# Kernel tuning notes

Hardware: AMD Instinct MI355X
Metric: run time of the kernel (lower is better)

Reference implementation:

```python
import jax, jax.numpy as jnp
import numpy as np
from jax import lax

A_RATIOS = (0.5, 1.0, 2.0)
A_SCALES = (8, 16, 32)
FEAT_STRIDE = 16
BASE_SIZE = 16
PRE_NMS = 6000     # n_test_pre_nms
POST_NMS = 300     # n_test_post_nms
NMS_THRESH = 0.7
MIN_SIZE = 16.0
SCALE = 1.0        # forward(scale=1.0) default
NEG = -1e10


def _anchor_base():
    # standard generate_anchor_base: centered at (8,8), ratios x scales
    py = px = BASE_SIZE / 2.0
    rows = []
    for r in A_RATIOS:
        for s in A_SCALES:
            h = BASE_SIZE * s * np.sqrt(r)
            w = BASE_SIZE * s * np.sqrt(1.0 / r)
            rows.append([py - h / 2.0, px - w / 2.0, py + h / 2.0, px + w / 2.0])
    return np.asarray(rows, np.float32)  # (A, 4)


def _all_anchors(height, width):
    base = jnp.asarray(_anchor_base())                                  # (A, 4)
    sy = (jnp.arange(height) * FEAT_STRIDE).astype(jnp.float32)
    sx = (jnp.arange(width) * FEAT_STRIDE).astype(jnp.float32)
    gy, gx = jnp.meshgrid(sy, sx, indexing='ij')
    shift = jnp.stack([gy.ravel(), gx.ravel(), gy.ravel(), gx.ravel()], axis=1)  # (K, 4)
    anch = base[None, :, :] + shift[:, None, :]                         # (K, A, 4)
    return anch.reshape(-1, 4)                                          # (K*A, 4)


def _conv(x, w, b, pad):
    y = lax.conv_general_dilated(x, w, (1, 1), [(pad, pad), (pad, pad)],
                                 dimension_numbers=('NCHW', 'OIHW', 'NCHW'))
    return y + b[None, :, None, None]


def _loc2bbox(anchors, locs):
    h = anchors[:, 2] - anchors[:, 0]
    w = anchors[:, 3] - anchors[:, 1]
    cy = anchors[:, 0] + 0.5 * h
    cx = anchors[:, 1] + 0.5 * w
    dy, dx, dh, dw = locs[:, 0], locs[:, 1], locs[:, 2], locs[:, 3]
    ncy = dy * h + cy
    ncx = dx * w + cx
    nh = jnp.exp(dh) * h
    nw = jnp.exp(dw) * w
    return jnp.stack([ncy - 0.5 * nh, ncx - 0.5 * nw,
                      ncy + 0.5 * nh, ncx + 0.5 * nw], axis=1)


def _iou_one_vs_all(box, boxes):
    ty = jnp.maximum(box[0], boxes[:, 0])
    tx = jnp.maximum(box[1], boxes[:, 1])
    by = jnp.minimum(box[2], boxes[:, 2])
    bx = jnp.minimum(box[3], boxes[:, 3])
    inter = jnp.maximum(by - ty, 0.0) * jnp.maximum(bx - tx, 0.0)
    a1 = (box[2] - box[0]) * (box[3] - box[1])
    a2 = (boxes[:, 2] - boxes[:, 0]) * (boxes[:, 3] - boxes[:, 1])
    return inter / (a1 + a2 - inter + 1e-9)


def _nms(boxes, scores):
    # greedy NMS with fixed POST_NMS output; invalid slots are zero boxes
    def step(s, _):
        i = jnp.argmax(s)
        valid = s[i] > NEG / 2
        ious = _iou_one_vs_all(boxes[i], boxes)
        s = jnp.where(ious > NMS_THRESH, NEG, s)  # suppresses self (iou=1)
        return s, (i, valid)
    _, (idx, valid) = lax.scan(step, scores, None, length=POST_NMS)
    return boxes[idx] * valid[:, None].astype(boxes.dtype)  # (POST_NMS, 4)


def _proposals(anchors, locs, fg, img_h, img_w):
    boxes = _loc2bbox(anchors, locs)
    boxes = jnp.stack([jnp.clip(boxes[:, 0], 0.0, img_h),
                       jnp.clip(boxes[:, 1], 0.0, img_w),
                       jnp.clip(boxes[:, 2], 0.0, img_h),
                       jnp.clip(boxes[:, 3], 0.0, img_w)], axis=1)
    hs = boxes[:, 2] - boxes[:, 0]
    ws = boxes[:, 3] - boxes[:, 1]
    ok = (hs >= MIN_SIZE * SCALE) & (ws >= MIN_SIZE * SCALE)
    sc = jnp.where(ok, fg, NEG)
    top_sc, idx = lax.top_k(sc, PRE_NMS)
    return _nms(boxes[idx], top_sc)


def reference(base_feat, W_conv1, b_conv1, W_score, b_score, W_loc, b_loc, img_h, img_w):
    N, _, H, W = base_feat.shape
    A = 9
    mid = jax.nn.relu(_conv(base_feat, W_conv1, b_conv1, 1))            # (N,512,H,W)
    rpn_locs = _conv(mid, W_loc, b_loc, 0).transpose(0, 2, 3, 1).reshape(N, H * W * A, 4)
    raw = _conv(mid, W_score, b_score, 0).transpose(0, 2, 3, 1)          # (N,H,W,2A)
    rpn_scores = raw.reshape(N, H * W * A, 2)
    fg = jax.nn.softmax(raw.reshape(N, H, W, A, 2), axis=-1)[..., 1].reshape(N, -1)
    anchors = _all_anchors(H, W)                                         # (H*W*A,4)
    ih, iw = float(img_h), float(img_w)
    prop = jax.vmap(lambda l, f: _proposals(anchors, l, f, ih, iw))(rpn_locs, fg)
    rois = prop.reshape(N * POST_NMS, 4)
    roi_indices = jnp.repeat(jnp.arange(N, dtype=jnp.int32), POST_NMS)
    return rpn_locs, rpn_scores, rois, roi_indices, anchors


def setup_inputs() -> dict:
    key = jax.random.key(0)
    k0, k1, k2, k3 = jax.random.split(key, 4)
    N, C, H, W = 4, 512, 64, 64
    nA = 9
    return {
        'base_feat': jax.random.normal(k0, (N, C, H, W), jnp.float32),
        'W_conv1': 0.01 * jax.random.normal(k1, (512, 512, 3, 3), jnp.float32),
        'b_conv1': jnp.zeros((512,), jnp.float32),
        'W_score': 0.01 * jax.random.normal(k2, (2 * nA, 512, 1, 1), jnp.float32),
        'b_score': jnp.zeros((2 * nA,), jnp.float32),
        'W_loc': 0.01 * jax.random.normal(k3, (4 * nA, 512, 1, 1), jnp.float32),
        'b_loc': jnp.zeros((4 * nA,), jnp.float32),
        'img_h': 1024,
        'img_w': 1024,
    }
```

## Files before the change

### kernel.cpp

```cpp
#include <hip/hip_runtime.h>
#include <math.h>

#define HH 64
#define WW 64
#define NIMG 4
#define CIN 512
#define AA 9
#define HWA (HH*WW*AA)
#define PRE_NMS 6000
#define POST_NMS 300
#define NEGV (-1e10f)
#define NEGK 0xD01502F9u
#define NWORD 94

#define OFF1 589824
#define OFF2 884736
#define OFF3 889536
#define OFF4 890736

typedef unsigned int u32;
typedef unsigned long long u64;
typedef _Float16 f16;
typedef _Float16 half8 __attribute__((ext_vector_type(8)));
typedef float f32x4 __attribute__((ext_vector_type(4)));

__device__ __forceinline__ void gload_lds16(const void* g, void* l)
{
    __builtin_amdgcn_global_load_lds((const __attribute__((address_space(1))) void*)g,
                                     (__attribute__((address_space(3))) void*)l,
                                     16, 0, 0);
}

__global__ __launch_bounds__(256) void k_prep_x(const float* __restrict__ x,
                                                f16* __restrict__ xh,
                                                f16* __restrict__ xl)
{
    __shared__ float tile[64][65];
    int ci0 = blockIdx.x * 64, y = blockIdx.y, n = blockIdx.z;
    int t = threadIdx.x;
    #pragma unroll
    for (int l = 0; l < 16; ++l) {
        int idx = l * 256 + t;
        int cc = idx >> 6, xc = idx & 63;
        tile[cc][xc] = x[((size_t)(n * CIN + ci0 + cc) * HH + y) * WW + xc];
    }
    __syncthreads();
    #pragma unroll
    for (int l = 0; l < 16; ++l) {
        int idx = l * 256 + t;
        int xc = idx >> 6, cc = idx & 63;
        float v = tile[cc][xc];
        f16 hi = (f16)v;
        f16 lo = (f16)(v - (float)hi);
        size_t o = ((size_t)(n * 64 + y) * 64 + xc) * 512 + ci0 + cc;
        xh[o] = hi; xl[o] = lo;
    }
}

__global__ __launch_bounds__(256) void k_prep_w(const float* __restrict__ W1,
                                                f16* __restrict__ wh,
                                                f16* __restrict__ wl)
{
    int idx = blockIdx.x * 256 + threadIdx.x;
    int co = idx >> 9, ci = idx & 511;
    #pragma unroll
    for (int tap = 0; tap < 9; ++tap) {
        float v = W1[(size_t)idx * 9 + tap];
        f16 hi = (f16)v;
        f16 lo = (f16)(v - (float)hi);
        size_t o = ((size_t)tap * 512 + co) * 512 + ci;
        wh[o] = hi; wl[o] = lo;
    }
}

__global__ __launch_bounds__(256, 4) void k_conv_mfma(const f16* __restrict__ xh,
                                                      const f16* __restrict__ xl,
                                                      const f16* __restrict__ wh,
                                                      const f16* __restrict__ wl,
                                                      const float* __restrict__ bias,
                                                      float* __restrict__ mid)
{
    __shared__ f16 sX[2][4][64][32];
    const int t = threadIdx.x;
    const int co0 = blockIdx.x * 64, yb = blockIdx.y, n = blockIdx.z;
    const int y0 = yb * 2;
    const int wv = t >> 6, lane = t & 63;
    const int q = lane >> 4, li = lane & 15;
    const int mh = wv & 1;
    const int xhp = wv >> 1;

    if (yb == 0 || yb == 31) {
        int rowu = (yb == 0) ? 0 : 3072;
        u32* p = (u32*)&sX[0][0][0][0];
        #pragma unroll
        for (int l = 0; l < 8; ++l) {
            int idx = l * 256 + t;
            int plane = idx >> 10, r = idx & 1023;
            p[plane * 4096 + rowu + r] = 0;
        }
    }

    f32x4 acc[2][2][2];
    #pragma unroll
    for (int mt = 0; mt < 2; ++mt)
        #pragma unroll
        for (int xn = 0; xn < 2; ++xn)
            #pragma unroll
            for (int yy = 0; yy < 2; ++yy)
                acc[mt][xn][yy] = (f32x4){0.f, 0.f, 0.f, 0.f};

    auto prefetch = [&](int ci0) {
        #pragma unroll
        for (int m = 0; m < 8; ++m) {
            int k2 = wv * 8 + m;
            int plane = k2 >> 4;
            int row = (k2 >> 2) & 3;
            int gy = y0 - 1 + row;
            if ((unsigned)gy < 64u) {
                int col = ((k2 & 3) << 4) + (lane >> 2);
                int s = lane & 3;
                const f16* src = (plane ? xl : xh) +
                    (((size_t)(n * 64 + gy) * 64 + col) * 512 + ci0 + s * 8);
                f16* dst = &sX[0][0][0][0] + (size_t)k2 * 512 + lane * 8;
                gload_lds16(src, dst);
            }
        }
    };

    half8 wa[2][2], wn[2][2];
    auto loadW = [&](half8 w[2][2], int ci0, int tap) {
        #pragma unroll
        for (int mt = 0; mt < 2; ++mt) {
            size_t base = ((size_t)(tap * 512) + co0 + mh * 32 + mt * 16 + li) * 512 + ci0 + q * 8;
            w[0][mt] = *(const half8*)(wh + base);
            w[1][mt] = *(const half8*)(wl + base);
        }
    };

    prefetch(0);
    loadW(wa, 0, 0);

    const half8 zero8 = {(f16)0, (f16)0, (f16)0, (f16)0, (f16)0, (f16)0, (f16)0, (f16)0};

    for (int chunk = 0; chunk < 16; ++chunk) {
        const int ci0 = chunk * 32;
        __syncthreads();

        #pragma unroll
        for (int tap = 0; tap < 9; ++tap) {
            if (tap < 8) loadW(wn, ci0, tap + 1);
            const int ky = tap / 3, kx = tap - ky * 3;

            half8 B[2][2][2];
            #pragma unroll
            for (int xn = 0; xn < 2; ++xn) {
                int xc = xhp * 32 + xn * 16 + li;
                int colr = xc + kx - 1;
                bool oob = (colr < 0) || (colr > 63);
                int colc = oob ? 0 : colr;
                #pragma unroll
                for (int yy = 0; yy < 2; ++yy) {
                    int row = yy + ky;
                    const f16* ph = &sX[0][row][colc][q * 8];
                    half8 vh = *(const half8*)ph;
                    half8 vl = *(const half8*)(ph + 8192);
                    if (oob) { vh = zero8; vl = zero8; }
                    B[0][xn][yy] = vh; B[1][xn][yy] = vl;
                }
            }
            #pragma unroll
            for (int mt = 0; mt < 2; ++mt)
                #pragma unroll
                for (int xn = 0; xn < 2; ++xn)
                    #pragma unroll
                    for (int yy = 0; yy < 2; ++yy)
                        acc[mt][xn][yy] = __builtin_amdgcn_mfma_f32_16x16x32_f16(wa[0][mt], B[0][xn][yy], acc[mt][xn][yy], 0, 0, 0);
            #pragma unroll
            for (int mt = 0; mt < 2; ++mt)
                #pragma unroll
                for (int xn = 0; xn < 2; ++xn)
                    #pragma unroll
                    for (int yy = 0; yy < 2; ++yy)
                        acc[mt][xn][yy] = __builtin_amdgcn_mfma_f32_16x16x32_f16(wa[0][mt], B[1][xn][yy], acc[mt][xn][yy], 0, 0, 0);
            #pragma unroll
            for (int mt = 0; mt < 2; ++mt)
                #pragma unroll
                for (int xn = 0; xn < 2; ++xn)
                    #pragma unroll
                    for (int yy = 0; yy < 2; ++yy)
                        acc[mt][xn][yy] = __builtin_amdgcn_mfma_f32_16x16x32_f16(wa[1][mt], B[0][xn][yy], acc[mt][xn][yy], 0, 0, 0);

            if (tap < 8) {
                #pragma unroll
                for (int pl = 0; pl < 2; ++pl)
                    #pragma unroll
                    for (int mt = 0; mt < 2; ++mt) wa[pl][mt] = wn[pl][mt];
            }
        }

        if (chunk + 1 < 16) {
            __syncthreads();
            prefetch(ci0 + 32);
            loadW(wa, ci0 + 32, 0);
        }
    }

    #pragma unroll
    for (int mt = 0; mt < 2; ++mt) {
        #pragma unroll
        for (int r = 0; r < 4; ++r) {
            int co = co0 + mh * 32 + mt * 16 + q * 4 + r;
            float bv = bias[co];
            #pragma unroll
            for (int xn = 0; xn < 2; ++xn) {
                int xc = xhp * 32 + xn * 16 + li;
                #pragma unroll
                for (int yy = 0; yy < 2; ++yy) {
                    float v = acc[mt][xn][yy][r] + bv;
                    mid[((size_t)(n * 512 + co) * HH + y0 + yy) * WW + xc] = v > 0.f ? v : 0.f;
                }
            }
        }
    }
}

__global__ __launch_bounds__(256) void k_htrans(const float* __restrict__ Ws,
                                                const float* __restrict__ Wl,
                                                float* __restrict__ Wt2)
{
    int i = blockIdx.x * 256 + threadIdx.x;
    if (i >= 512 * 64) return;
    int ci = i >> 6, co = i & 63;
    float v = 0.f;
    if (co < 18) v = Ws[co * 512 + ci];
    else if (co < 54) v = Wl[(co - 18) * 512 + ci];
    Wt2[i] = v;
}

__global__ __launch_bounds__(256) void k_hgemm(const float* __restrict__ mid,
                                               const float* __restrict__ Wt2,
                                               float* __restrict__ sraw)
{
    __shared__ float sM[32][64];
    __shared__ float sW2[32][64];
    const int t = threadIdx.x;
    const int px0 = blockIdx.x * 64, n = blockIdx.y;
    const int tx = t & 15, ty = t >> 4;

    float acc[4][4];
    #pragma unroll
    for (int c = 0; c < 4; ++c)
        #pragma unroll
        for (int j = 0; j < 4; ++j) acc[c][j] = 0.f;

    for (int ci0 = 0; ci0 < 512; ci0 += 32) {
        __syncthreads();
        #pragma unroll
        for (int l = 0; l < 8; ++l) {
            int i = l * 256 + t;
            int ci = i >> 6, px = i & 63;
            sM[ci][px] = mid[((size_t)n * 512 + ci0 + ci) * 4096 + px0 + px];
            sW2[ci][px] = Wt2[(size_t)(ci0 + ci) * 64 + px];
        }
        __syncthreads();
        #pragma unroll
        for (int ci = 0; ci < 32; ++ci) {
            float mv[4], wv[4];
            #pragma unroll
            for (int j = 0; j < 4; ++j) mv[j] = sM[ci][tx * 4 + j];
            #pragma unroll
            for (int c = 0; c < 4; ++c) wv[c] = sW2[ci][ty * 4 + c];
            #pragma unroll
            for (int c = 0; c < 4; ++c)
                #pragma unroll
                for (int j = 0; j < 4; ++j) acc[c][j] += wv[c] * mv[j];
        }
    }
    #pragma unroll
    for (int c = 0; c < 4; ++c) {
        float4 v = make_float4(acc[c][0], acc[c][1], acc[c][2], acc[c][3]);
        *(float4*)&sraw[((size_t)n * 64 + ty * 4 + c) * 4096 + px0 + tx * 4] = v;
    }
}

__global__ __launch_bounds__(256) void k_decode(const float* __restrict__ sraw,
                                                const float* __restrict__ bsc,
                                                const float* __restrict__ blc,
                                                const int* __restrict__ ph,
                                                const int* __restrict__ pw,
                                                float* __restrict__ out,
                                                float* __restrict__ boxes,
                                                u32* __restrict__ key)
{
    int p = blockIdx.x * 256 + threadIdx.x;
    int n = p >> 12, pi = p & 4095;
    int y = pi >> 6, xq = pi & 63;

    const float* S = sraw + (size_t)n * 64 * 4096 + pi;
    float* o0 = out + (size_t)n * 147456;
    float* o1 = out + OFF1 + (size_t)n * 73728;
    float IHf = (float)(*ph), IWf = (float)(*pw);

    #pragma unroll
    for (int a = 0; a < 9; ++a) {
        float s0 = S[(size_t)(2 * a) * 4096] + bsc[2 * a];
        float s1 = S[(size_t)(2 * a + 1) * 4096] + bsc[2 * a + 1];
        float dy = S[(size_t)(18 + 4 * a) * 4096] + blc[4 * a];
        float dx = S[(size_t)(19 + 4 * a) * 4096] + blc[4 * a + 1];
        float dh = S[(size_t)(20 + 4 * a) * 4096] + blc[4 * a + 2];
        float dw = S[(size_t)(21 + 4 * a) * 4096] + blc[4 * a + 3];

        o1[(pi * 9 + a) * 2 + 0] = s0;
        o1[(pi * 9 + a) * 2 + 1] = s1;
        o0[(pi * 9 + a) * 4 + 0] = dy;
        o0[(pi * 9 + a) * 4 + 1] = dx;
        o0[(pi * 9 + a) * 4 + 2] = dh;
        o0[(pi * 9 + a) * 4 + 3] = dw;

        float mm = fmaxf(s0, s1);
        float e0 = expf(s0 - mm), e1 = expf(s1 - mm);
        float fg = e1 / (e0 + e1);

        int ri = a / 3, si = a - ri * 3;
        double s = (double)(8 << si);
        double rr = (ri == 0) ? 0.5 : ((ri == 1) ? 1.0 : 2.0);
        double hh = 16.0 * s * sqrt(rr);
        double wd = 16.0 * s * sqrt(1.0 / rr);
        float a0 = (float)(8.0 - hh * 0.5) + (float)(y * 16);
        float a1 = (float)(8.0 - wd * 0.5) + (float)(xq * 16);
        float a2 = (float)(8.0 + hh * 0.5) + (float)(y * 16);
        float a3 = (float)(8.0 + wd * 0.5) + (float)(xq * 16);

        float h = a2 - a0, w = a3 - a1;
        float cy = a0 + 0.5f * h, cx = a1 + 0.5f * w;
        float ncy = dy * h + cy, ncx = dx * w + cx;
        float nh = expf(dh) * h, nw = expf(dw) * w;
        float b0 = fminf(fmaxf(ncy - 0.5f * nh, 0.f), IHf);
        float b1 = fminf(fmaxf(ncx - 0.5f * nw, 0.f), IWf);
        float b2 = fminf(fmaxf(ncy + 0.5f * nh, 0.f), IHf);
        float b3 = fminf(fmaxf(ncx + 0.5f * nw, 0.f), IWf);

        bool ok = (b2 - b0 >= 16.0f) && (b3 - b1 >= 16.0f);
        float sc = ok ? fg : NEGV;

        int gi = n * HWA + pi * 9 + a;
        ((float4*)boxes)[gi] = make_float4(b0, b1, b2, b3);
        u32 u = __float_as_uint(sc);
        u32 kasc = (u & 0x80000000u) ? ~u : (u | 0x80000000u);
        key[gi] = ~kasc;
    }
}

__global__ void k_misc(float* __restrict__ out)
{
    int i = blockIdx.x * 256 + threadIdx.x;
    if (i < 4800) out[OFF2 + i] = 0.f;
    if (i < 1200) out[OFF3 + i] = (float)(i / 300);
    if (i < HWA) {
        int pi = i / 9, a = i - pi * 9;
        int y = pi >> 6, xq = pi & 63;
        int ri = a / 3, si = a - ri * 3;
        double s = (double)(8 << si);
        double rr = (ri == 0) ? 0.5 : ((ri == 1) ? 1.0 : 2.0);
        double hh = 16.0 * s * sqrt(rr);
        double wd = 16.0 * s * sqrt(1.0 / rr);
        out[OFF4 + i * 4 + 0] = (float)(8.0 - hh * 0.5) + (float)(y * 16);
        out[OFF4 + i * 4 + 1] = (float)(8.0 - wd * 0.5) + (float)(xq * 16);
        out[OFF4 + i * 4 + 2] = (float)(8.0 + hh * 0.5) + (float)(y * 16);
        out[OFF4 + i * 4 + 3] = (float)(8.0 + wd * 0.5) + (float)(xq * 16);
    }
}

__global__ __launch_bounds__(1024) void k_select(const u32* __restrict__ key,
                                                 u64* __restrict__ cmp,
                                                 int* __restrict__ nvalid)
{
    __shared__ int hist[256];
    __shared__ u32 sPref;
    __shared__ int sR;
    __shared__ int cLess, cEq, cVal;
    int n = blockIdx.x, t = threadIdx.x;
    const u32* k0 = key + (size_t)n * HWA;

    u32 pref = 0, mask = 0;
    int R = PRE_NMS;
    for (int pass = 0; pass < 4; ++pass) {
        int shift = 24 - pass * 8;
        if (t < 256) hist[t] = 0;
        __syncthreads();
        for (int i = t; i < HWA; i += 1024) {
            u32 k = k0[i];
            if ((k & mask) == pref) atomicAdd(&hist[(k >> shift) & 255], 1);
        }
        __syncthreads();
        if (t == 0) {
            int cum = 0;
            for (int b = 0; b < 256; ++b) {
                int c = hist[b];
                if (cum + c >= R) { sPref = pref | ((u32)b << shift); sR = R - cum; break; }
                cum += c;
            }
        }
        __syncthreads();
        pref = sPref; R = sR; mask |= (0xFFu << shift);
        __syncthreads();
    }
    u32 T = pref;
    if (t == 0) { cLess = 0; cEq = 0; cVal = 0; }
    __syncthreads();
    for (int i = t; i < HWA; i += 1024) {
        u32 k = k0[i];
        if (k < NEGK) atomicAdd(&cVal, 1);
        if (k < T) {
            int p = atomicAdd(&cLess, 1);
            cmp[(size_t)n * 8192 + p] = ((u64)k << 32) | (u32)i;
        } else if (k == T) {
            int p = atomicAdd(&cEq, 1);
            if (p < R) cmp[(size_t)n * 8192 + (PRE_NMS - 1 - p)] = ((u64)k << 32) | (u32)i;
        }
    }
    for (int i = PRE_NMS + t; i < 8192; i += 1024) cmp[(size_t)n * 8192 + i] = ~0ull;
    __syncthreads();
    if (t == 0) nvalid[n] = cVal < PRE_NMS ? cVal : PRE_NMS;
}

__global__ __launch_bounds__(1024) void k_sort(const u64* __restrict__ cmp,
                                               const float* __restrict__ boxes,
                                               float* __restrict__ boxesS)
{
    __shared__ u64 sK[8192];
    int n = blockIdx.x, t = threadIdx.x;
    for (int i = t; i < 8192; i += 1024) sK[i] = cmp[(size_t)n * 8192 + i];
    for (unsigned k = 2; k <= 8192; k <<= 1) {
        for (unsigned j = k >> 1; j > 0; j >>= 1) {
            __syncthreads();
            #pragma unroll
            for (int v = 0; v < 8; ++v) {
                int i = v * 1024 + t;
                int ixj = i ^ (int)j;
                if (ixj > i) {
                    u64 a = sK[i], b = sK[ixj];
                    bool up = ((i & (int)k) == 0);
                    if (up ? (a > b) : (a < b)) { sK[i] = b; sK[ixj] = a; }
                }
            }
        }
    }
    __syncthreads();
    const float4* bsrc = (const float4*)boxes + (size_t)n * HWA;
    float4* bdst = (float4*)boxesS + (size_t)n * PRE_NMS;
    for (int i = t; i < PRE_NMS; i += 1024) {
        u32 idx = (u32)(sK[i] & 0xFFFFFFFFu);
        bdst[i] = bsrc[idx];
    }
}

__global__ __launch_bounds__(64) void k_iou(const float* __restrict__ boxesS,
                                            u64* __restrict__ mask)
{
    __shared__ float4 cb[64];
    int w = blockIdx.x, ic = blockIdx.y, n = blockIdx.z;
    if (w < ic) return;
    int t = threadIdx.x;
    const float4* B = (const float4*)boxesS + (size_t)n * PRE_NMS;
    int jc = w * 64 + t;
    cb[t] = (jc < PRE_NMS) ? B[jc] : make_float4(0.f, 0.f, 0.f, 0.f);
    __syncthreads();
    int i = ic * 64 + t;
    if (i >= PRE_NMS) return;
    float4 bb = B[i];
    float area1 = (bb.z - bb.x) * (bb.w - bb.y);
    u64 m = 0;
    #pragma unroll 8
    for (int j = 0; j < 64; ++j) {
        float4 o = cb[j];
        float ty_ = fmaxf(bb.x, o.x), tx_ = fmaxf(bb.y, o.y);
        float by_ = fminf(bb.z, o.z), bx_ = fminf(bb.w, o.w);
        float inter = fmaxf(by_ - ty_, 0.f) * fmaxf(bx_ - tx_, 0.f);
        float area2 = (o.z - o.x) * (o.w - o.y);
        float iou = inter / (area1 + area2 - inter + 1e-9f);
        if (iou > 0.7f) m |= (1ull << j);
    }
    mask[((size_t)n * PRE_NMS + i) * NWORD + w] = m;
}

__global__ __launch_bounds__(64) void k_nms3(const u64* __restrict__ mask,
                                             const int* __restrict__ nvalid,
                                             const float* __restrict__ boxesS,
                                             float* __restrict__ rois)
{
    int n = blockIdx.x, lane = threadIdx.x;
    int nv = nvalid[n];
    const u64* M = mask + (size_t)n * PRE_NMS * NWORD;
    const float4* B = (const float4*)boxesS + (size_t)n * PRE_NMS;

    auto vmask = [&](int w) -> u64 {
        int lo = w * 64;
        if (nv >= lo + 64) return ~0ull;
        if (nv <= lo) return 0ull;
        return (1ull << (nv - lo)) - 1ull;
    };
    u64 vm0 = vmask(lane);
    u64 vm1 = (lane < NWORD - 64) ? vmask(64 + lane) : 0ull;
    u64 rem0 = 0, rem1 = 0;

    int cnt = 0;
    while (cnt < POST_NMS) {
        u64 c0 = (~rem0) & vm0;
        u64 c1 = (~rem1) & vm1;
        int sel;
        u64 b0 = __ballot(c0 != 0);
        if (b0) {
            int l = __builtin_ctzll(b0);
            u64 w = __shfl(c0, l);
            sel = l * 64 + __builtin_ctzll(w);
        } else {
            u64 b1 = __ballot(c1 != 0);
            if (!b1) break;
            int l = __builtin_ctzll(b1);
            u64 w = __shfl(c1, l);
            sel = (64 + l) * 64 + __builtin_ctzll(w);
        }
        if (lane == 0) {
            float4 bb = B[sel];
            float* orow = rois + (size_t)(n * POST_NMS + cnt) * 4;
            orow[0] = bb.x; orow[1] = bb.y; orow[2] = bb.z; orow[3] = bb.w;
        }
        const u64* Mr = M + (size_t)sel * NWORD;
        rem0 |= Mr[lane];
        if (lane < NWORD - 64) rem1 |= Mr[64 + lane];
        cnt++;
    }
}

extern "C" void kernel_launch(void* const* d_in, const int* in_sizes, int n_in,
                              void* d_out, int out_size, void* d_ws, size_t ws_size,
                              hipStream_t stream)
{
    const float* x  = (const float*)d_in[0];
    const float* W1 = (const float*)d_in[1];
    const float* b1 = (const float*)d_in[2];
    const float* Ws = (const float*)d_in[3];
    const float* bs = (const float*)d_in[4];
    const float* Wl = (const float*)d_in[5];
    const float* bl = (const float*)d_in[6];
    const int* ih   = (const int*)d_in[7];
    const int* iw   = (const int*)d_in[8];
    float* out = (float*)d_out;
    char* ws = (char*)d_ws;

    f16*   Wh2    = (f16*)  (ws);
    f16*   Wl2    = (f16*)  (ws + 4718592);
    float* mid    = (float*)(ws + 9437184);
    f16*   xh     = (f16*)  (ws + 42991616);
    f16*   xl     = (f16*)  (ws + 59768832);
    float* boxes  = (float*)(ws + 42991616);
    u32*   key    = (u32*)  (ws + 45350912);
    u64*   cmp    = (u64*)  (ws + 45940736);
    float* boxesS = (float*)(ws + 46202880);
    int*   nval   = (int*)  (ws + 46586880);
    float* Wt2    = (float*)(ws);
    float* sraw   = (float*)(ws + 262144);
    u64*   iomask = (u64*)  (ws + 9437184);

    k_prep_x<<<dim3(8, 64, 4), 256, 0, stream>>>(x, xh, xl);
    k_prep_w<<<1024, 256, 0, stream>>>(W1, Wh2, Wl2);
    k_conv_mfma<<<dim3(8, 32, 4), 256, 0, stream>>>(xh, xl, Wh2, Wl2, b1, mid);
    k_htrans<<<128, 256, 0, stream>>>(Ws, Wl, Wt2);
    k_hgemm<<<dim3(64, 4), 256, 0, stream>>>(mid, Wt2, sraw);
    k_decode<<<64, 256, 0, stream>>>(sraw, bs, bl, ih, iw, out, boxes, key);
    k_misc<<<144, 256, 0, stream>>>(out);
    k_select<<<4, 1024, 0, stream>>>(key, cmp, nval);
    k_sort<<<4, 1024, 0, stream>>>(cmp, boxes, boxesS);
    k_iou<<<dim3(NWORD, NWORD, NIMG), 64, 0, stream>>>(boxesS, iomask);
    k_nms3<<<NIMG, 64, 0, stream>>>(iomask, nval, boxesS, out + OFF2);
}
```

Baseline: 862.9 us.

## Replace bitonic sort with rank scatter, batch NMS candidates, swap conv grid order

The 4-block bitonic sort over 8192 keys is replaced by a rank kernel where each of 6000 threads per image counts smaller keys and scatters its box to that rank. This spreads the work over many blocks instead of four heavily synchronised ones, at the cost of O(n^2) global reads. The NMS loop now gathers up to 8 candidate indices and prefetches their mask rows together, so memory latency is paid once per batch rather than once per kept box. The conv grid is also transposed so consecutive blocks walk row tiles before output-channel tiles, which changes L2 reuse of the weights and inputs.

```diff
diff --git a/kernel.cpp b/kernel.cpp
--- a/kernel.cpp
+++ b/kernel.cpp
@@ -82,7 +82,7 @@
 {
     __shared__ f16 sX[2][4][64][32];
     const int t = threadIdx.x;
-    const int co0 = blockIdx.x * 64, yb = blockIdx.y, n = blockIdx.z;
+    const int yb = blockIdx.x, co0 = blockIdx.y * 64, n = blockIdx.z;
     const int y0 = yb * 2;
     const int wv = t >> 6, lane = t & 63;
     const int q = lane >> 4, li = lane & 15;
@@ -419,40 +419,26 @@
             if (p < R) cmp[(size_t)n * 8192 + (PRE_NMS - 1 - p)] = ((u64)k << 32) | (u32)i;
         }
     }
-    for (int i = PRE_NMS + t; i < 8192; i += 1024) cmp[(size_t)n * 8192 + i] = ~0ull;
     __syncthreads();
     if (t == 0) nvalid[n] = cVal < PRE_NMS ? cVal : PRE_NMS;
 }
 
-__global__ __launch_bounds__(1024) void k_sort(const u64* __restrict__ cmp,
-                                               const float* __restrict__ boxes,
-                                               float* __restrict__ boxesS)
-{
-    __shared__ u64 sK[8192];
-    int n = blockIdx.x, t = threadIdx.x;
-    for (int i = t; i < 8192; i += 1024) sK[i] = cmp[(size_t)n * 8192 + i];
-    for (unsigned k = 2; k <= 8192; k <<= 1) {
-        for (unsigned j = k >> 1; j > 0; j >>= 1) {
-            __syncthreads();
-            #pragma unroll
-            for (int v = 0; v < 8; ++v) {
-                int i = v * 1024 + t;
-                int ixj = i ^ (int)j;
-                if (ixj > i) {
-                    u64 a = sK[i], b = sK[ixj];
-                    bool up = ((i & (int)k) == 0);
-                    if (up ? (a > b) : (a < b)) { sK[i] = b; sK[ixj] = a; }
-                }
-            }
-        }
-    }
-    __syncthreads();
-    const float4* bsrc = (const float4*)boxes + (size_t)n * HWA;
-    float4* bdst = (float4*)boxesS + (size_t)n * PRE_NMS;
-    for (int i = t; i < PRE_NMS; i += 1024) {
-        u32 idx = (u32)(sK[i] & 0xFFFFFFFFu);
-        bdst[i] = bsrc[idx];
-    }
+__global__ __launch_bounds__(64) void k_rank(const u64* __restrict__ cmp,
+                                             const float* __restrict__ boxes,
+                                             float* __restrict__ boxesS)
+{
+    int n = blockIdx.y;
+    int i = blockIdx.x * 64 + threadIdx.x;
+    if (i >= PRE_NMS) return;
+    const u64* K = cmp + (size_t)n * 8192;
+    u64 ki = K[i];
+    int rank = 0;
+    #pragma unroll 8
+    for (int j = 0; j < PRE_NMS; ++j)
+        rank += (K[j] < ki) ? 1 : 0;
+    u32 idx = (u32)(ki & 0xFFFFFFFFu);
+    ((float4*)boxesS)[(size_t)n * PRE_NMS + rank] =
+        ((const float4*)boxes)[(size_t)n * HWA + idx];
 }
 
 __global__ __launch_bounds__(64) void k_iou(const float* __restrict__ boxesS,
@@ -484,7 +470,7 @@
     mask[((size_t)n * PRE_NMS + i) * NWORD + w] = m;
 }
 
-__global__ __launch_bounds__(64) void k_nms3(const u64* __restrict__ mask,
+__global__ __launch_bounds__(64) void k_nms4(const u64* __restrict__ mask,
                                              const int* __restrict__ nvalid,
                                              const float* __restrict__ boxesS,
                                              float* __restrict__ rois)
@@ -506,30 +492,55 @@
 
     int cnt = 0;
     while (cnt < POST_NMS) {
-        u64 c0 = (~rem0) & vm0;
-        u64 c1 = (~rem1) & vm1;
-        int sel;
-        u64 b0 = __ballot(c0 != 0);
-        if (b0) {
-            int l = __builtin_ctzll(b0);
-            u64 w = __shfl(c0, l);
-            sel = l * 64 + __builtin_ctzll(w);
-        } else {
-            u64 b1 = __ballot(c1 != 0);
-            if (!b1) break;
-            int l = __builtin_ctzll(b1);
-            u64 w = __shfl(c1, l);
-            sel = (64 + l) * 64 + __builtin_ctzll(w);
-        }
-        if (lane == 0) {
-            float4 bb = B[sel];
-            float* orow = rois + (size_t)(n * POST_NMS + cnt) * 4;
-            orow[0] = bb.x; orow[1] = bb.y; orow[2] = bb.z; orow[3] = bb.w;
-        }
-        const u64* Mr = M + (size_t)sel * NWORD;
-        rem0 |= Mr[lane];
-        if (lane < NWORD - 64) rem1 |= Mr[64 + lane];
-        cnt++;
+        u64 t0 = (~rem0) & vm0;
+        u64 t1 = (~rem1) & vm1;
+        int cand[8];
+        int nc = 0;
+        #pragma unroll
+        for (int k = 0; k < 8; ++k) {
+            u64 b0 = __ballot(t0 != 0);
+            int c = -1;
+            if (b0) {
+                int l = __builtin_ctzll(b0);
+                u64 w = __shfl(t0, l);
+                c = l * 64 + __builtin_ctzll(w);
+                if (lane == l) t0 &= t0 - 1;
+            } else {
+                u64 b1 = __ballot(t1 != 0);
+                if (b1) {
+                    int l = __builtin_ctzll(b1);
+                    u64 w = __shfl(t1, l);
+                    c = (64 + l) * 64 + __builtin_ctzll(w);
+                    if (lane == l) t1 &= t1 - 1;
+                }
+            }
+            if (c < 0) break;
+            cand[nc++] = c;
+        }
+        if (nc == 0) break;
+
+        u64 r0[8], r1[8];
+        for (int k = 0; k < nc; ++k) {
+            const u64* Mr = M + (size_t)cand[k] * NWORD;
+            r0[k] = Mr[lane];
+            r1[k] = (lane < NWORD - 64) ? Mr[64 + lane] : 0ull;
+        }
+
+        for (int k = 0; k < nc && cnt < POST_NMS; ++k) {
+            int c = cand[k];
+            int w = c >> 6, b = c & 63;
+            u64 cw = (w < 64) ? __shfl(rem0, w) : __shfl(rem1, w - 64);
+            if (!((cw >> b) & 1ull)) {
+                if (lane == 0) {
+                    float4 bb = B[c];
+                    float* orow = rois + (size_t)(n * POST_NMS + cnt) * 4;
+                    orow[0] = bb.x; orow[1] = bb.y; orow[2] = bb.z; orow[3] = bb.w;
+                }
+                rem0 |= r0[k];
+                rem1 |= r1[k];
+                cnt++;
+            }
+        }
     }
 }
 
@@ -565,13 +576,13 @@
 
     k_prep_x<<<dim3(8, 64, 4), 256, 0, stream>>>(x, xh, xl);
     k_prep_w<<<1024, 256, 0, stream>>>(W1, Wh2, Wl2);
-    k_conv_mfma<<<dim3(8, 32, 4), 256, 0, stream>>>(xh, xl, Wh2, Wl2, b1, mid);
+    k_conv_mfma<<<dim3(32, 8, 4), 256, 0, stream>>>(xh, xl, Wh2, Wl2, b1, mid);
     k_htrans<<<128, 256, 0, stream>>>(Ws, Wl, Wt2);
     k_hgemm<<<dim3(64, 4), 256, 0, stream>>>(mid, Wt2, sraw);
     k_decode<<<64, 256, 0, stream>>>(sraw, bs, bl, ih, iw, out, boxes, key);
     k_misc<<<144, 256, 0, stream>>>(out);
     k_select<<<4, 1024, 0, stream>>>(key, cmp, nval);
-    k_sort<<<4, 1024, 0, stream>>>(cmp, boxes, boxesS);
+    k_rank<<<dim3(94, NIMG), 64, 0, stream>>>(cmp, boxes, boxesS);
     k_iou<<<dim3(NWORD, NWORD, NIMG), 64, 0, stream>>>(boxesS, iomask);
-    k_nms3<<<NIMG, 64, 0, stream>>>(iomask, nval, boxesS, out + OFF2);
-}
+    k_nms4<<<NIMG, 64, 0, stream>>>(iomask, nval, boxesS, out + OFF2);
+}
```

New measurement: 1.035 ms. +19.9%, slower.
